# Kernel tuning notes

Measured on AMD Instinct MI355X. Metric: run time of the kernel, lower is better.

## Reference

```python
import jax, jax.numpy as jnp
import numpy as np

P = 8  # patch size (fixed in module)


def setup_inputs() -> dict:
    key = jax.random.key(0)
    k0, k1, k2, k3 = jax.random.split(key, 4)
    d, B, H, W = 64, 4, 256, 256
    x = jax.random.normal(k0, (B, d, H, W), dtype=jnp.float32)
    # conv weights (bias=False). 1x1 convs stored as [out, in]; depthwise as [out,1,3,3]
    w1 = jax.random.normal(k1, (6 * d, d), dtype=jnp.float32) * 0.05
    w_dw = jax.random.normal(k2, (6 * d, 1, 3, 3), dtype=jnp.float32) * 0.1
    w_out = jax.random.normal(k3, (d, 2 * d), dtype=jnp.float32) * 0.05
    ln_w = jnp.ones((2 * d,), dtype=jnp.float32)
    ln_b = jnp.zeros((2 * d,), dtype=jnp.float32)
    return {"x": x, "w1": w1, "w_dw": w_dw, "w_out": w_out, "ln_w": ln_w, "ln_b": ln_b}


def _to_patches(t):
    # [b,c,H,W] -> [b,c,H/P,W/P,P,P]
    b, c, h, w = t.shape
    return t.reshape(b, c, h // P, P, w // P, P).transpose(0, 1, 2, 4, 3, 5)


def reference(x, w1, w_dw, w_out, ln_w, ln_b):
    B, C, H, W = x.shape
    # to_hidden: 1x1 conv, dim -> 6*dim
    hidden = jnp.einsum('bchw,oc->bohw', x, w1)
    # to_hidden_dw: depthwise 3x3, groups = 6*dim
    hidden = jax.lax.conv_general_dilated(
        hidden, w_dw, window_strides=(1, 1), padding='SAME',
        feature_group_count=w_dw.shape[0],
        dimension_numbers=('NCHW', 'OIHW', 'NCHW'))
    q, k, v = jnp.split(hidden, 3, axis=1)  # each [B, 2C, H, W]
    # patch-wise frequency-domain correlation: irfft2(rfft2(q) * rfft2(k))
    qf = jnp.fft.rfft2(_to_patches(q))
    kf = jnp.fft.rfft2(_to_patches(k))
    out = jnp.fft.irfft2(qf * kf, s=(P, P))  # [B,2C,H/P,W/P,P,P]
    b, c = out.shape[:2]
    out = out.transpose(0, 1, 2, 4, 3, 5).reshape(b, c, H, W)
    # LayerNorm (WithBias) over the channel dim, eps=1e-5, biased variance
    mu = out.mean(axis=1, keepdims=True)
    var = out.var(axis=1, keepdims=True)
    out = (out - mu) / jnp.sqrt(var + 1e-5) * ln_w[None, :, None, None] + ln_b[None, :, None, None]
    # gate by v, then project_out: 1x1 conv, 2*dim -> dim
    out = v * out
    return jnp.einsum('bchw,oc->bohw', out, w_out)
```

## Files before the change

kernel.cpp:

```cpp
#include <hip/hip_runtime.h>

#define NTHREADS 512

#define NB   4
#define HH   256
#define WW   256

#define XF     0
#define HIDA   8192
#define HIDB   0
#define Q_U    15872
#define K_U    24064
#define V_U    32256
#define CORRU  0
#define REDU   8192
#define BFRU   24064
#define PBUFU  0
#define MU_U   40448
#define RS_U   40576
#define SMEM_U 40704

typedef short s16x8 __attribute__((ext_vector_type(8)));
typedef float f32x16 __attribute__((ext_vector_type(16)));
typedef _Float16 h16x8 __attribute__((ext_vector_type(8)));
typedef _Float16 h16x4 __attribute__((ext_vector_type(4)));
typedef _Float16 h16x2 __attribute__((ext_vector_type(2)));

__device__ inline unsigned short f2bf(float f) {
    unsigned u = __builtin_bit_cast(unsigned, f);
    u += 0x7FFFu + ((u >> 16) & 1u);
    return (unsigned short)(u >> 16);
}
__device__ inline float bf2f(unsigned short s) {
    return __builtin_bit_cast(float, (unsigned)s << 16);
}
__device__ inline unsigned short f2h(float f) {
    _Float16 h = (_Float16)f;
    return __builtin_bit_cast(unsigned short, h);
}

__device__ inline float fdot2(unsigned a, unsigned b, float c) {
#if __has_builtin(__builtin_amdgcn_fdot2)
    return __builtin_amdgcn_fdot2(__builtin_bit_cast(h16x2, a),
                                  __builtin_bit_cast(h16x2, b), c, false);
#else
    h16x2 av = __builtin_bit_cast(h16x2, a);
    h16x2 bv = __builtin_bit_cast(h16x2, b);
    return c + (float)av[0] * (float)bv[0] + (float)av[1] * (float)bv[1];
#endif
}

__global__ __launch_bounds__(256)
void fsas_prepack(const float* __restrict__ w1, const float* __restrict__ wout,
                  unsigned short* __restrict__ ws)
{
    int t = blockIdx.x * 256 + threadIdx.x;
    if (t < 24576) {
        int b = t & 7, ln = (t >> 3) & 63, ks = (t >> 9) & 3, mtc = t >> 11;
        int l32 = ln & 31, half = ln >> 5;
        int o = mtc * 32 + l32;
        int kk = ks * 16 + half * 8 + b;
        ws[t] = f2bf(w1[o * 64 + kk]);
    } else if (t < 40960) {
        int idx = t - 24576;
        int lo = idx >= 8192;
        if (lo) idx -= 8192;
        int b = idx & 7, ln = (idx >> 3) & 63, ks = (idx >> 9) & 7, mtp = idx >> 12;
        int l32 = ln & 31, half = ln >> 5;
        int o = mtp * 32 + l32;
        int kk = ks * 16 + half * 8 + b;
        float v = wout[o * 128 + kk];
        unsigned short hi = f2bf(v);
        ws[t] = lo ? f2bf(v - bf2f(hi)) : hi;
    }
}

__global__ __launch_bounds__(NTHREADS, 4)
void fsas_fused(const float* __restrict__ x,
                const float* __restrict__ wdw,
                const unsigned short* __restrict__ wsu,
                const float* __restrict__ lnw,
                const float* __restrict__ lnb,
                float* __restrict__ out)
{
    __shared__ unsigned short su[SMEM_U];

    const int tid = threadIdx.x;
    const int wv  = tid >> 6;
    const int ln  = tid & 63;
    const int l32 = ln & 31, half = ln >> 5;
    const int lin  = (blockIdx.z * 32 + blockIdx.y) * 32 + blockIdx.x;
    const int orig = (lin & 7) * 512 + (lin >> 3);
    const int pw = orig & 31;
    const int ph = (orig >> 5) & 31;
    const int b  = orig >> 10;
    const int h0  = ph * 8;
    const int w0  = pw * 8;

    for (int idx = tid; idx < 8192; idx += NTHREADS) {
        int c = idx >> 7, pos = idx & 127;
        float v = 0.f;
        if (pos < 100) {
            int r = pos / 10, q = pos - r * 10;
            int h = h0 - 1 + r, w = w0 - 1 + q;
            if ((unsigned)h < (unsigned)HH && (unsigned)w < (unsigned)WW)
                v = x[((b * 64 + c) * HH + h) * WW + w];
        }
        int lane = (pos & 31) + 32 * ((c >> 3) & 1);
        int nt = pos >> 5, ks = c >> 4, bb = c & 7;
        su[XF + ((nt * 4 + ks) * 64 + lane) * 8 + bb] = f2bf(v);
    }
    __syncthreads();

    const s16x8* waf = (const s16x8*)wsu;
    const int mt2 = wv & 1, nt = (wv >> 1) & 3;
    const int pos = nt * 32 + l32;
    const int r10 = pos / 10, c10 = pos - r10 * 10;
    const int posoff = r10 * 12 + c10;
    const bool pvalid = pos < 100;

    s16x8 breg[4];
#pragma unroll
    for (int ks = 0; ks < 4; ++ks)
        breg[ks] = *(const s16x8*)(su + XF + ((nt * 4 + ks) * 64 + ln) * 8);

#pragma unroll 2
    for (int rnd = 0; rnd < 6; ++rnd) {
        const int hid_base = (rnd & 1) ? HIDB : HIDA;
        {
            int mtc = rnd * 2 + mt2;
            f32x16 acc = {};
#pragma unroll
            for (int ks = 0; ks < 4; ++ks) {
                s16x8 afr = waf[(mtc * 4 + ks) * 64 + ln];
                acc = __builtin_amdgcn_mfma_f32_32x32x16_bf16(afr, breg[ks], acc, 0, 0, 0);
            }
            if (pvalid) {
#pragma unroll
                for (int rr = 0; rr < 16; ++rr) {
                    int o_l = mt2 * 32 + (rr & 3) + 8 * (rr >> 2) + 4 * half;
                    su[hid_base + o_l * 120 + posoff] = f2h(acc[rr]);
                }
            }
        }
        __syncthreads();
        {
            int oc = tid >> 3, py = tid & 7;
            const float* wr = wdw + (rnd * 64 + oc) * 9;
            float wgt[9];
#pragma unroll
            for (int t = 0; t < 9; ++t) wgt[t] = wr[t];
            const unsigned short* hb = su + hid_base + oc * 120 + py * 12;
            _Float16 hh[3][12];
#pragma unroll
            for (int rr = 0; rr < 3; ++rr) {
                uint2 ua = *(const uint2*)(hb + rr * 12);
                uint2 ub = *(const uint2*)(hb + rr * 12 + 4);
                uint2 uc = *(const uint2*)(hb + rr * 12 + 8);
                h16x4 a = __builtin_bit_cast(h16x4, ua);
                h16x4 bq = __builtin_bit_cast(h16x4, ub);
                h16x4 cq = __builtin_bit_cast(h16x4, uc);
#pragma unroll
                for (int t = 0; t < 4; ++t) { hh[rr][t] = a[t]; hh[rr][4 + t] = bq[t]; hh[rr][8 + t] = cq[t]; }
            }
            float o_[8];
#pragma unroll
            for (int px = 0; px < 8; ++px) {
                o_[px] = wgt[0] * (float)hh[0][px] + wgt[1] * (float)hh[0][px + 1] + wgt[2] * (float)hh[0][px + 2]
                       + wgt[3] * (float)hh[1][px] + wgt[4] * (float)hh[1][px + 1] + wgt[5] * (float)hh[1][px + 2]
                       + wgt[6] * (float)hh[2][px] + wgt[7] * (float)hh[2][px + 1] + wgt[8] * (float)hh[2][px + 2];
            }
            int buf = rnd >> 1;
            int cb  = (rnd & 1) * 64 + oc;
            int cs  = cb & 7;
            unsigned short* dst = su + Q_U + buf * 8192 + cb * 64 + ((py ^ cs) * 8);
            uint4 o4;
            o4.x = (unsigned)f2h(o_[0]) | ((unsigned)f2h(o_[1]) << 16);
            o4.y = (unsigned)f2h(o_[2]) | ((unsigned)f2h(o_[3]) << 16);
            o4.z = (unsigned)f2h(o_[4]) | ((unsigned)f2h(o_[5]) << 16);
            o4.w = (unsigned)f2h(o_[6]) | ((unsigned)f2h(o_[7]) << 16);
            *(uint4*)dst = o4;
        }
    }
    __syncthreads();

    {
        int c = tid >> 2, i0 = tid & 3, cs = c & 7;
        const unsigned short* qr = su + Q_U + c * 64;
        const unsigned short* kr = su + K_U + c * 64;
        float o0[8] = {0.f,0.f,0.f,0.f,0.f,0.f,0.f,0.f};
        float o1[8] = {0.f,0.f,0.f,0.f,0.f,0.f,0.f,0.f};
#pragma unroll
        for (int a = 0; a < 8; ++a) {
            uint4 uq = *(const uint4*)(qr + ((a ^ cs) * 8));
            int k0 = (i0 - a) & 7, k1 = (i0 + 4 - a) & 7;
            uint4 uk0 = *(const uint4*)(kr + ((k0 ^ cs) * 8));
            uint4 uk1 = *(const uint4*)(kr + ((k1 ^ cs) * 8));
            unsigned qw[4]  = {uq.x,  uq.y,  uq.z,  uq.w};
            unsigned kw0[4] = {uk0.x, uk0.y, uk0.z, uk0.w};
            unsigned kw1[4] = {uk1.x, uk1.y, uk1.z, uk1.w};
            unsigned kr0[8], kr1[8];
#pragma unroll
            for (int p = 0; p < 4; ++p) {
                kr0[2 * p]     = __builtin_amdgcn_perm(kw0[(p + 3) & 3], kw0[p], 0x07060100u);
                kr0[2 * p + 1] = __builtin_amdgcn_alignbit(kw0[p], kw0[p], 16);
                kr1[2 * p]     = __builtin_amdgcn_perm(kw1[(p + 3) & 3], kw1[p], 0x07060100u);
                kr1[2 * p + 1] = __builtin_amdgcn_alignbit(kw1[p], kw1[p], 16);
            }
#pragma unroll
            for (int j = 0; j < 8; ++j) {
#pragma unroll
                for (int p = 0; p < 4; ++p) {
                    o0[j] = fdot2(qw[p], kr0[(j - 2 * p) & 7], o0[j]);
                    o1[j] = fdot2(qw[p], kr1[(j - 2 * p) & 7], o1[j]);
                }
            }
        }
        uint4 a4, b4;
        a4.x = (unsigned)f2h(o0[0]) | ((unsigned)f2h(o0[1]) << 16);
        a4.y = (unsigned)f2h(o0[2]) | ((unsigned)f2h(o0[3]) << 16);
        a4.z = (unsigned)f2h(o0[4]) | ((unsigned)f2h(o0[5]) << 16);
        a4.w = (unsigned)f2h(o0[6]) | ((unsigned)f2h(o0[7]) << 16);
        b4.x = (unsigned)f2h(o1[0]) | ((unsigned)f2h(o1[1]) << 16);
        b4.y = (unsigned)f2h(o1[2]) | ((unsigned)f2h(o1[3]) << 16);
        b4.z = (unsigned)f2h(o1[4]) | ((unsigned)f2h(o1[5]) << 16);
        b4.w = (unsigned)f2h(o1[6]) | ((unsigned)f2h(o1[7]) << 16);
        *(uint4*)(su + CORRU + c * 64 + ((i0 ^ cs) * 8)) = a4;
        *(uint4*)(su + CORRU + c * 64 + (((i0 + 4) ^ cs) * 8)) = b4;
    }
    __syncthreads();

    {
        float* redF = (float*)(su + REDU);
        int px = tid & 63, grp = tid >> 6;
        int prow = px >> 3, pcol = px & 7;
        float s = 0.f, s2 = 0.f;
#pragma unroll
        for (int i = 0; i < 16; ++i) {
            int c = i * 8 + grp;
            float v = (float)__builtin_bit_cast(_Float16,
                        su[CORRU + c * 64 + ((prow ^ (c & 7)) * 8) + pcol]);
            s += v; s2 += v * v;
        }
        redF[grp * 64 + px] = s;
        redF[512 + grp * 64 + px] = s2;
    }
    __syncthreads();
    if (tid < 64) {
        float* redF = (float*)(su + REDU);
        float s = 0.f, s2 = 0.f;
#pragma unroll
        for (int g = 0; g < 8; ++g) {
            s  += redF[g * 64 + tid];
            s2 += redF[512 + g * 64 + tid];
        }
        float m = s * (1.f / 128.f);
        float var = s2 * (1.f / 128.f) - m * m;
        ((float*)(su + MU_U))[tid] = m;
        ((float*)(su + RS_U))[tid] = rsqrtf(var + 1e-5f);
    }
    __syncthreads();

    {
        int py = tid & 7, c0 = (tid >> 3) * 2;
        const float* muF = (const float*)(su + MU_U);
        const float* rsF = (const float*)(su + RS_U);
        float4 m0 = *(const float4*)(muF + py * 8);
        float4 m1 = *(const float4*)(muF + py * 8 + 4);
        float4 r0 = *(const float4*)(rsF + py * 8);
        float4 r1 = *(const float4*)(rsF + py * 8 + 4);
        float mm[8] = {m0.x, m0.y, m0.z, m0.w, m1.x, m1.y, m1.z, m1.w};
        float rr[8] = {r0.x, r0.y, r0.z, r0.w, r1.x, r1.y, r1.z, r1.w};
#pragma unroll
        for (int cc = 0; cc < 2; ++cc) {
            int c = c0 + cc, cs = c & 7;
            uint4 cu = *(const uint4*)(su + CORRU + c * 64 + ((py ^ cs) * 8));
            uint4 vu = *(const uint4*)(su + V_U   + c * 64 + ((py ^ cs) * 8));
            h16x8 ch = __builtin_bit_cast(h16x8, cu);
            h16x8 vh = __builtin_bit_cast(h16x8, vu);
            float wc = lnw[c], bc = lnb[c];
            int base = BFRU + (((py >> 2) * 8 + (c >> 4)) * 64 + 8 * (py & 3) + 32 * ((c >> 3) & 1)) * 8 + (c & 7);
#pragma unroll
            for (int j = 0; j < 8; ++j) {
                float t = (((float)ch[j] - mm[j]) * rr[j] * wc + bc) * (float)vh[j];
                su[base + j * 8] = f2bf(t);
            }
        }
    }
    __syncthreads();

    {
        int kseg = wv & 1, mtp = (wv >> 1) & 1, ntp = wv >> 2;
        const s16x8* whi = (const s16x8*)(wsu + 24576);
        const s16x8* wlo = (const s16x8*)(wsu + 32768);
        f32x16 acc = {};
#pragma unroll
        for (int k2 = 0; k2 < 4; ++k2) {
            int ks = kseg * 4 + k2;
            s16x8 ah = whi[(mtp * 8 + ks) * 64 + ln];
            s16x8 al = wlo[(mtp * 8 + ks) * 64 + ln];
            s16x8 bfr = *(const s16x8*)(su + BFRU + ((ntp * 8 + ks) * 64 + ln) * 8);
            acc = __builtin_amdgcn_mfma_f32_32x32x16_bf16(ah, bfr, acc, 0, 0, 0);
            acc = __builtin_amdgcn_mfma_f32_32x32x16_bf16(al, bfr, acc, 0, 0, 0);
        }
        float* pbufF = (float*)(su + PBUFU);
        int seg = (ntp * 2 + mtp) * 2 + kseg;
#pragma unroll
        for (int r = 0; r < 16; ++r)
            pbufF[r * 544 + seg * 68 + ln] = acc[r];
    }
    __syncthreads();

    {
        const float* pbufF = (const float*)(su + PBUFU);
#pragma unroll
        for (int it = 0; it < 2; ++it) {
            int u = tid + it * NTHREADS;
            int o = u >> 4, pg = u & 15;
            int mtp = o >> 5, row = o & 31;
            int rg = row >> 3, rem = row & 7, hf = rem >> 2, ii = rem & 3;
            int r = rg * 4 + ii;
            int px0 = pg * 4;
            int ntp = px0 >> 5;
            int lane0 = (px0 & 31) + 32 * hf;
            const float* pb = pbufF + r * 544 + ((ntp * 2 + mtp) * 2) * 68 + lane0;
            float4 s0 = *(const float4*)(pb);
            float4 s1 = *(const float4*)(pb + 68);
            float4 rr;
            rr.x = s0.x + s1.x; rr.y = s0.y + s1.y;
            rr.z = s0.z + s1.z; rr.w = s0.w + s1.w;
            int py = px0 >> 3, wx = px0 & 7;
            *(float4*)(out + (((size_t)(b * 64 + o) * HH) + h0 + py) * WW + w0 + wx) = rr;
        }
    }
}

extern "C" void kernel_launch(void* const* d_in, const int* in_sizes, int n_in,
                              void* d_out, int out_size, void* d_ws, size_t ws_size,
                              hipStream_t stream) {
    const float* x    = (const float*)d_in[0];
    const float* w1   = (const float*)d_in[1];
    const float* wdw  = (const float*)d_in[2];
    const float* wout = (const float*)d_in[3];
    const float* lnw  = (const float*)d_in[4];
    const float* lnb  = (const float*)d_in[5];
    float* o = (float*)d_out;
    unsigned short* ws = (unsigned short*)d_ws;

    fsas_prepack<<<160, 256, 0, stream>>>(w1, wout, ws);
    dim3 grid(32, 32, NB);
    fsas_fused<<<grid, dim3(NTHREADS), 0, stream>>>(x, wdw, ws, lnw, lnb, o);
}
```

Measured before the change: 298.6 us.

## Shrink LDS footprint by keeping v in registers and dropping split-K reduction buffer

Each block now uses a single hidden buffer and holds the v channels in registers instead of shared memory. The correlation work is remapped so each thread handles one output row for two channels, matching the depthwise thread mapping. The final projection runs on only four waves with full K per wave, writing directly to global memory without a partial-sum buffer. Shared memory drops from about 80KB to about 50KB per block, which should allow more resident blocks. In exchange the barrier count goes up, the final stage leaves half the waves idle, and the global stores become scalar rather than float4.

```diff
diff --git a/kernel.cpp b/kernel.cpp
--- a/kernel.cpp
+++ b/kernel.cpp
@@ -7,18 +7,15 @@
 #define WW   256
 
 #define XF     0
-#define HIDA   8192
-#define HIDB   0
-#define Q_U    15872
-#define K_U    24064
-#define V_U    32256
+#define HIDA   0
+#define Q_U    8192
+#define K_U    16384
 #define CORRU  0
 #define REDU   8192
-#define BFRU   24064
-#define PBUFU  0
-#define MU_U   40448
-#define RS_U   40576
-#define SMEM_U 40704
+#define BFRU   8192
+#define MU_U   24576
+#define RS_U   24704
+#define SMEM_U 24832
 
 typedef short s16x8 __attribute__((ext_vector_type(8)));
 typedef float f32x16 __attribute__((ext_vector_type(16)));
@@ -123,10 +120,13 @@
 #pragma unroll
     for (int ks = 0; ks < 4; ++ks)
         breg[ks] = *(const s16x8*)(su + XF + ((nt * 4 + ks) * 64 + ln) * 8);
-
-#pragma unroll 2
+    __syncthreads();
+
+    uint4 vA, vB;
+    const int dw_oc = tid >> 3, dw_py = tid & 7;
+
+#pragma unroll
     for (int rnd = 0; rnd < 6; ++rnd) {
-        const int hid_base = (rnd & 1) ? HIDB : HIDA;
         {
             int mtc = rnd * 2 + mt2;
             f32x16 acc = {};
@@ -139,18 +139,18 @@
 #pragma unroll
                 for (int rr = 0; rr < 16; ++rr) {
                     int o_l = mt2 * 32 + (rr & 3) + 8 * (rr >> 2) + 4 * half;
-                    su[hid_base + o_l * 120 + posoff] = f2h(acc[rr]);
+                    su[HIDA + o_l * 120 + posoff] = f2h(acc[rr]);
                 }
             }
         }
         __syncthreads();
         {
-            int oc = tid >> 3, py = tid & 7;
+            int oc = dw_oc, py = dw_py;
             const float* wr = wdw + (rnd * 64 + oc) * 9;
             float wgt[9];
 #pragma unroll
             for (int t = 0; t < 9; ++t) wgt[t] = wr[t];
-            const unsigned short* hb = su + hid_base + oc * 120 + py * 12;
+            const unsigned short* hb = su + HIDA + oc * 120 + py * 12;
             _Float16 hh[3][12];
 #pragma unroll
             for (int rr = 0; rr < 3; ++rr) {
@@ -170,63 +170,61 @@
                        + wgt[3] * (float)hh[1][px] + wgt[4] * (float)hh[1][px + 1] + wgt[5] * (float)hh[1][px + 2]
                        + wgt[6] * (float)hh[2][px] + wgt[7] * (float)hh[2][px + 1] + wgt[8] * (float)hh[2][px + 2];
             }
-            int buf = rnd >> 1;
-            int cb  = (rnd & 1) * 64 + oc;
-            int cs  = cb & 7;
-            unsigned short* dst = su + Q_U + buf * 8192 + cb * 64 + ((py ^ cs) * 8);
             uint4 o4;
             o4.x = (unsigned)f2h(o_[0]) | ((unsigned)f2h(o_[1]) << 16);
             o4.y = (unsigned)f2h(o_[2]) | ((unsigned)f2h(o_[3]) << 16);
             o4.z = (unsigned)f2h(o_[4]) | ((unsigned)f2h(o_[5]) << 16);
             o4.w = (unsigned)f2h(o_[6]) | ((unsigned)f2h(o_[7]) << 16);
-            *(uint4*)dst = o4;
-        }
+            if (rnd < 4) {
+                int buf = rnd >> 1;
+                int cb  = (rnd & 1) * 64 + oc;
+                int cs  = cb & 7;
+                *(uint4*)(su + Q_U + buf * 8192 + cb * 64 + ((py ^ cs) * 8)) = o4;
+            } else if (rnd == 4) {
+                vA = o4;
+            } else {
+                vB = o4;
+            }
+        }
+        if (rnd < 5) __syncthreads();
     }
     __syncthreads();
 
     {
-        int c = tid >> 2, i0 = tid & 3, cs = c & 7;
-        const unsigned short* qr = su + Q_U + c * 64;
-        const unsigned short* kr = su + K_U + c * 64;
-        float o0[8] = {0.f,0.f,0.f,0.f,0.f,0.f,0.f,0.f};
-        float o1[8] = {0.f,0.f,0.f,0.f,0.f,0.f,0.f,0.f};
-#pragma unroll
-        for (int a = 0; a < 8; ++a) {
-            uint4 uq = *(const uint4*)(qr + ((a ^ cs) * 8));
-            int k0 = (i0 - a) & 7, k1 = (i0 + 4 - a) & 7;
-            uint4 uk0 = *(const uint4*)(kr + ((k0 ^ cs) * 8));
-            uint4 uk1 = *(const uint4*)(kr + ((k1 ^ cs) * 8));
-            unsigned qw[4]  = {uq.x,  uq.y,  uq.z,  uq.w};
-            unsigned kw0[4] = {uk0.x, uk0.y, uk0.z, uk0.w};
-            unsigned kw1[4] = {uk1.x, uk1.y, uk1.z, uk1.w};
-            unsigned kr0[8], kr1[8];
-#pragma unroll
-            for (int p = 0; p < 4; ++p) {
-                kr0[2 * p]     = __builtin_amdgcn_perm(kw0[(p + 3) & 3], kw0[p], 0x07060100u);
-                kr0[2 * p + 1] = __builtin_amdgcn_alignbit(kw0[p], kw0[p], 16);
-                kr1[2 * p]     = __builtin_amdgcn_perm(kw1[(p + 3) & 3], kw1[p], 0x07060100u);
-                kr1[2 * p + 1] = __builtin_amdgcn_alignbit(kw1[p], kw1[p], 16);
-            }
-#pragma unroll
-            for (int j = 0; j < 8; ++j) {
+        int oc = dw_oc, py = dw_py;
+#pragma unroll
+        for (int cc = 0; cc < 2; ++cc) {
+            int c = oc + cc * 64, cs = c & 7;
+            const unsigned short* qr = su + Q_U + c * 64;
+            const unsigned short* kr = su + K_U + c * 64;
+            float o0[8] = {0.f,0.f,0.f,0.f,0.f,0.f,0.f,0.f};
+#pragma unroll
+            for (int a = 0; a < 8; ++a) {
+                uint4 uq = *(const uint4*)(qr + ((a ^ cs) * 8));
+                int k0 = (py - a) & 7;
+                uint4 uk = *(const uint4*)(kr + ((k0 ^ cs) * 8));
+                unsigned qw[4] = {uq.x, uq.y, uq.z, uq.w};
+                unsigned kw[4] = {uk.x, uk.y, uk.z, uk.w};
+                unsigned kr0[8];
 #pragma unroll
                 for (int p = 0; p < 4; ++p) {
-                    o0[j] = fdot2(qw[p], kr0[(j - 2 * p) & 7], o0[j]);
-                    o1[j] = fdot2(qw[p], kr1[(j - 2 * p) & 7], o1[j]);
+                    kr0[2 * p]     = __builtin_amdgcn_perm(kw[(p + 3) & 3], kw[p], 0x07060100u);
+                    kr0[2 * p + 1] = __builtin_amdgcn_alignbit(kw[p], kw[p], 16);
                 }
-            }
-        }
-        uint4 a4, b4;
-        a4.x = (unsigned)f2h(o0[0]) | ((unsigned)f2h(o0[1]) << 16);
-        a4.y = (unsigned)f2h(o0[2]) | ((unsigned)f2h(o0[3]) << 16);
-        a4.z = (unsigned)f2h(o0[4]) | ((unsigned)f2h(o0[5]) << 16);
-        a4.w = (unsigned)f2h(o0[6]) | ((unsigned)f2h(o0[7]) << 16);
-        b4.x = (unsigned)f2h(o1[0]) | ((unsigned)f2h(o1[1]) << 16);
-        b4.y = (unsigned)f2h(o1[2]) | ((unsigned)f2h(o1[3]) << 16);
-        b4.z = (unsigned)f2h(o1[4]) | ((unsigned)f2h(o1[5]) << 16);
-        b4.w = (unsigned)f2h(o1[6]) | ((unsigned)f2h(o1[7]) << 16);
-        *(uint4*)(su + CORRU + c * 64 + ((i0 ^ cs) * 8)) = a4;
-        *(uint4*)(su + CORRU + c * 64 + (((i0 + 4) ^ cs) * 8)) = b4;
+#pragma unroll
+                for (int j = 0; j < 8; ++j) {
+#pragma unroll
+                    for (int p = 0; p < 4; ++p)
+                        o0[j] = fdot2(qw[p], kr0[(j - 2 * p) & 7], o0[j]);
+                }
+            }
+            uint4 a4;
+            a4.x = (unsigned)f2h(o0[0]) | ((unsigned)f2h(o0[1]) << 16);
+            a4.y = (unsigned)f2h(o0[2]) | ((unsigned)f2h(o0[3]) << 16);
+            a4.z = (unsigned)f2h(o0[4]) | ((unsigned)f2h(o0[5]) << 16);
+            a4.w = (unsigned)f2h(o0[6]) | ((unsigned)f2h(o0[7]) << 16);
+            *(uint4*)(su + CORRU + c * 64 + ((py ^ cs) * 8)) = a4;
+        }
     }
     __syncthreads();
 
@@ -262,7 +260,7 @@
     __syncthreads();
 
     {
-        int py = tid & 7, c0 = (tid >> 3) * 2;
+        int oc = dw_oc, py = dw_py;
         const float* muF = (const float*)(su + MU_U);
         const float* rsF = (const float*)(su + RS_U);
         float4 m0 = *(const float4*)(muF + py * 8);
@@ -273,11 +271,10 @@
         float rr[8] = {r0.x, r0.y, r0.z, r0.w, r1.x, r1.y, r1.z, r1.w};
 #pragma unroll
         for (int cc = 0; cc < 2; ++cc) {
-            int c = c0 + cc, cs = c & 7;
+            int c = oc + cc * 64, cs = c & 7;
             uint4 cu = *(const uint4*)(su + CORRU + c * 64 + ((py ^ cs) * 8));
-            uint4 vu = *(const uint4*)(su + V_U   + c * 64 + ((py ^ cs) * 8));
             h16x8 ch = __builtin_bit_cast(h16x8, cu);
-            h16x8 vh = __builtin_bit_cast(h16x8, vu);
+            h16x8 vh = __builtin_bit_cast(h16x8, cc ? vB : vA);
             float wc = lnw[c], bc = lnb[c];
             int base = BFRU + (((py >> 2) * 8 + (c >> 4)) * 64 + 8 * (py & 3) + 32 * ((c >> 3) & 1)) * 8 + (c & 7);
 #pragma unroll
@@ -289,48 +286,26 @@
     }
     __syncthreads();
 
-    {
-        int kseg = wv & 1, mtp = (wv >> 1) & 1, ntp = wv >> 2;
+    if (wv < 4) {
+        int mtp = wv & 1, ntp = wv >> 1;
         const s16x8* whi = (const s16x8*)(wsu + 24576);
         const s16x8* wlo = (const s16x8*)(wsu + 32768);
-        f32x16 acc = {};
-#pragma unroll
-        for (int k2 = 0; k2 < 4; ++k2) {
-            int ks = kseg * 4 + k2;
-            s16x8 ah = whi[(mtp * 8 + ks) * 64 + ln];
-            s16x8 al = wlo[(mtp * 8 + ks) * 64 + ln];
+        f32x16 acc_h = {}, acc_l = {};
+#pragma unroll
+        for (int ks = 0; ks < 8; ++ks) {
+            s16x8 ah  = whi[(mtp * 8 + ks) * 64 + ln];
+            s16x8 al  = wlo[(mtp * 8 + ks) * 64 + ln];
             s16x8 bfr = *(const s16x8*)(su + BFRU + ((ntp * 8 + ks) * 64 + ln) * 8);
-            acc = __builtin_amdgcn_mfma_f32_32x32x16_bf16(ah, bfr, acc, 0, 0, 0);
-            acc = __builtin_amdgcn_mfma_f32_32x32x16_bf16(al, bfr, acc, 0, 0, 0);
-        }
-        float* pbufF = (float*)(su + PBUFU);
-        int seg = (ntp * 2 + mtp) * 2 + kseg;
-#pragma unroll
-        for (int r = 0; r < 16; ++r)
-            pbufF[r * 544 + seg * 68 + ln] = acc[r];
-    }
-    __syncthreads();
-
-    {
-        const float* pbufF = (const float*)(su + PBUFU);
-#pragma unroll
-        for (int it = 0; it < 2; ++it) {
-            int u = tid + it * NTHREADS;
-            int o = u >> 4, pg = u & 15;
-            int mtp = o >> 5, row = o & 31;
-            int rg = row >> 3, rem = row & 7, hf = rem >> 2, ii = rem & 3;
-            int r = rg * 4 + ii;
-            int px0 = pg * 4;
-            int ntp = px0 >> 5;
-            int lane0 = (px0 & 31) + 32 * hf;
-            const float* pb = pbufF + r * 544 + ((ntp * 2 + mtp) * 2) * 68 + lane0;
-            float4 s0 = *(const float4*)(pb);
-            float4 s1 = *(const float4*)(pb + 68);
-            float4 rr;
-            rr.x = s0.x + s1.x; rr.y = s0.y + s1.y;
-            rr.z = s0.z + s1.z; rr.w = s0.w + s1.w;
-            int py = px0 >> 3, wx = px0 & 7;
-            *(float4*)(out + (((size_t)(b * 64 + o) * HH) + h0 + py) * WW + w0 + wx) = rr;
+            acc_h = __builtin_amdgcn_mfma_f32_32x32x16_bf16(ah, bfr, acc_h, 0, 0, 0);
+            acc_l = __builtin_amdgcn_mfma_f32_32x32x16_bf16(al, bfr, acc_l, 0, 0, 0);
+        }
+        int px = ntp * 32 + l32;
+        int py = px >> 3, wx = px & 7;
+#pragma unroll
+        for (int r = 0; r < 16; ++r) {
+            int row = (r >> 2) * 8 + half * 4 + (r & 3);
+            int o = mtp * 32 + row;
+            out[(((size_t)(b * 64 + o) * HH) + h0 + py) * WW + w0 + wx] = acc_h[r] + acc_l[r];
         }
     }
 }
```

Result: slower. 314.9 us (+5.5%).
